# Kernel optimization log

Hardware: AMD Instinct MI355X
Metric: run time of the kernel (lower is better)

Reference implementation:

```python
import jax, jax.numpy as jnp
import numpy as np

TWO_PI = 2.0 * np.pi
B, S_IN, S_OUT, K, HID = 1024, 4096, 4096, 8, 512
EPS = 1e-6


def setup_inputs() -> dict:
    key = jax.random.key(0)
    k1, k2, k3, k4, k5, k6, k7, k8 = jax.random.split(key, 8)
    x_in = jax.random.uniform(k1, (B, S_OUT), dtype=jnp.float32) * TWO_PI
    x_passive = jax.random.normal(k2, (B, S_IN), dtype=jnp.float32)
    log_density = jax.random.normal(k3, (B, 1), dtype=jnp.float32)
    # MLP params (nn.Linear default-ish init scale)
    lim1 = 1.0 / np.sqrt(S_IN)
    lim2 = 1.0 / np.sqrt(HID)
    w1 = jax.random.uniform(k4, (S_IN, HID), jnp.float32, -lim1, lim1)
    b1 = jax.random.uniform(k5, (HID,), jnp.float32, -lim1, lim1)
    w2 = jax.random.uniform(k6, (HID, S_OUT * 3 * K), jnp.float32, -lim2, lim2)
    b2 = jax.random.uniform(k7, (S_OUT * 3 * K,), jnp.float32, -lim2, lim2)
    phase_shift = jax.random.uniform(k8, (1,), jnp.float32)
    return {"x_in": x_in, "x_passive": x_passive, "log_density": log_density,
            "w1": w1, "b1": b1, "w2": w2, "b2": b2, "phase_shift": phase_shift}


def reference(x_in, x_passive, log_density, w1, b1, w2, b2, phase_shift):
    # normalise network input with global mean / (unbiased) std, as torch does
    xn = (x_passive - x_passive.mean()) / x_passive.std(ddof=1)
    # dense network: Linear -> tanh -> Linear -> tanh (final_activation=activation)
    net = jnp.tanh(jnp.tanh(xn @ w1 + b1) @ w2 + b2)            # (B, S*3K)
    net = net.reshape(-1, S_OUT, 3 * K)
    h_raw, w_raw, d_raw = net[..., :K], net[..., K:2 * K], net[..., 2 * K:]
    h_norm = jax.nn.softmax(h_raw, axis=2) * TWO_PI              # (B,S,K)
    w_norm = jax.nn.softmax(w_raw, axis=2) * TWO_PI
    d_norm = jax.nn.softplus(d_raw)
    bshape = (h_norm.shape[0], S_OUT, 1)
    x_kp = jnp.concatenate([jnp.full(bshape, -EPS, h_norm.dtype),
                            jnp.cumsum(w_norm, axis=2)], axis=2)  # (B,S,K+1)
    phi_kp = jnp.concatenate([jnp.zeros(bshape, h_norm.dtype),
                              jnp.cumsum(h_norm, axis=2)], axis=2)
    x = x_in[..., None]                                          # (B,S,1)
    # searchsorted (left) per element: count of knots strictly less than x, minus 1
    k_ind = jnp.sum(x_kp < x, axis=2, keepdims=True) - 1         # (B,S,1) int
    k_ind = jnp.clip(k_ind, 0, K - 1)
    g = lambda a, i: jnp.take_along_axis(a, i, axis=2)
    w_k = g(w_norm, k_ind)
    h_k = g(h_norm, k_ind)
    s_k = h_k / w_k
    d_k = g(d_norm, k_ind)
    d_kp1 = g(d_norm, (k_ind + 1) % K)
    x_km1 = g(x_kp, k_ind)
    phi_km1 = g(phi_kp, k_ind)
    alpha = (x - x_km1) / w_k
    a1m = alpha * (1.0 - alpha)
    denom = s_k + (d_kp1 + d_k - 2.0 * s_k) * a1m
    phi_out = (phi_km1 + h_k * (s_k * alpha ** 2 + d_k * a1m) / denom)[..., 0]
    phi_out = (phi_out + phase_shift) % TWO_PI                   # (B,S)
    grad = s_k ** 2 * (d_kp1 * alpha ** 2 + 2.0 * s_k * a1m
                       + d_k * (1.0 - alpha) ** 2) / denom ** 2  # (B,S,1)
    log_density = log_density - jnp.log(grad).sum(axis=1)        # (B,1)
    return phi_out, log_density
```

## Files before the change

kernel.cpp:

```cpp
#include <hip/hip_runtime.h>
#include <cstdint>
#include <cstddef>


typedef unsigned short u16;
typedef __bf16 bf16x8 __attribute__((ext_vector_type(8)));
typedef float f32x4 __attribute__((ext_vector_type(4)));
typedef unsigned short u16x8 __attribute__((ext_vector_type(8)));
typedef unsigned short u16x4 __attribute__((ext_vector_type(4)));
typedef unsigned short u16x2 __attribute__((ext_vector_type(2)));

#define TWOPI_F 6.28318530717958647692f

static __device__ __forceinline__ u16 f32_to_bf16(float f){
  unsigned u = __builtin_bit_cast(unsigned, f);
  return (u16)((u + 0x7fffu + ((u >> 16) & 1u)) >> 16);
}
static __device__ __forceinline__ void async16(void* lds, const void* g){
  __builtin_amdgcn_global_load_lds((const __attribute__((address_space(1))) void*)g,
                                   (__attribute__((address_space(3))) void*)lds,
                                   16, 0, 0);
}
static __device__ __forceinline__ float fast_tanh(float x){
  x = fminf(fmaxf(x, -15.f), 15.f);
  float e = __expf(2.f * x);
  return (e - 1.f) / (e + 1.f);
}
static __device__ __forceinline__ float softplus_f(float x){
  return fmaxf(x, 0.f) + __logf(1.f + __expf(-fabsf(x)));
}

__global__ void k_stats(const float* __restrict__ xp, float* __restrict__ stats){
  __shared__ float ss[4], sq[4];
  const int tid = threadIdx.x;
  const long gt = (long)blockIdx.x * 256 + tid;
  const float4* x4 = (const float4*)xp;
  float s = 0.f, q = 0.f;
  #pragma unroll
  for (int p = 0; p < 4; ++p){
    float4 v = x4[gt + (long)p * 262144];
    s += v.x + v.y + v.z + v.w;
    q += v.x*v.x + v.y*v.y + v.z*v.z + v.w*v.w;
  }
  #pragma unroll
  for (int off = 32; off; off >>= 1){
    s += __shfl_down(s, off);
    q += __shfl_down(q, off);
  }
  if ((tid & 63) == 0){ ss[tid>>6] = s; sq[tid>>6] = q; }
  __syncthreads();
  if (tid == 0){
    atomicAdd(stats,     ss[0]+ss[1]+ss[2]+ss[3]);
    atomicAdd(stats + 1, sq[0]+sq[1]+sq[2]+sq[3]);
  }
}

__global__ void k_prep(const float* __restrict__ xp, const float* __restrict__ stats,
                       u16* __restrict__ xn){
  const long t = (long)blockIdx.x * 256 + threadIdx.x;
  const float sum = stats[0], sq = stats[1];
  const float N = 4194304.f;
  const float mean = sum / N;
  const float istd = rsqrtf((sq - sum*sum/N) / (N - 1.f));
  const float4* x4 = (const float4*)xp;
  const float4 a = x4[2*t], b = x4[2*t+1];
  u16x8 o;
  o[0]=f32_to_bf16((a.x-mean)*istd); o[1]=f32_to_bf16((a.y-mean)*istd);
  o[2]=f32_to_bf16((a.z-mean)*istd); o[3]=f32_to_bf16((a.w-mean)*istd);
  o[4]=f32_to_bf16((b.x-mean)*istd); o[5]=f32_to_bf16((b.y-mean)*istd);
  o[6]=f32_to_bf16((b.z-mean)*istd); o[7]=f32_to_bf16((b.w-mean)*istd);
  ((u16x8*)xn)[t] = o;
}

__global__ __launch_bounds__(256) void k_transpose_cvt(const float* __restrict__ in,
                                                       u16* __restrict__ out,
                                                       int Kd, int Nd){
  __shared__ __align__(16) u16 tT[128*256];
  const int tid = threadIdx.x;
  const long k0 = (long)blockIdx.x * 256, n0 = (long)blockIdx.y * 128;
  const int lam = tid & 31, g = tid >> 5;
  const int c = lam * 4;
  const int sig = (lam & 7) << 2;
  #pragma unroll
  for (int pass = 0; pass < 16; ++pass){
    const int P = pass*8 + g;
    const float4 f0 = *(const float4*)&in[(k0 + 2*P    )*Nd + n0 + c];
    const float4 f1 = *(const float4*)&in[(k0 + 2*P + 1)*Nd + n0 + c];
    const int pp = 2*(P ^ sig);
    *(u16x2*)&tT[(c    )*256 + pp] = u16x2{f32_to_bf16(f0.x), f32_to_bf16(f1.x)};
    *(u16x2*)&tT[(c + 1)*256 + pp] = u16x2{f32_to_bf16(f0.y), f32_to_bf16(f1.y)};
    *(u16x2*)&tT[(c + 2)*256 + pp] = u16x2{f32_to_bf16(f0.z), f32_to_bf16(f1.z)};
    *(u16x2*)&tT[(c + 3)*256 + pp] = u16x2{f32_to_bf16(f0.w), f32_to_bf16(f1.w)};
  }
  __syncthreads();
  const int w = tid >> 6, l = tid & 63;
  const int lh = l >> 5, lk = l & 31;
  #pragma unroll
  for (int it = 0; it < 16; ++it){
    const int n = (w << 5) + (it << 1) + lh;
    const int s2 = (n >> 2) & 7;
    const u16x8 v = *(const u16x8*)&tT[n*256 + 8*(lk ^ s2)];
    *(u16x8*)&out[(n0 + n)*Kd + k0 + 8*lk] = v;
  }
}

__global__ __launch_bounds__(256, 2) void k_gemm1(
    const u16* __restrict__ xn,
    const u16* __restrict__ w1t,
    float* __restrict__ pp)
{
  __shared__ __align__(16) u16 sA[64*32];
  __shared__ __align__(16) u16 sB[64*32];
  const int tid = threadIdx.x, lane = tid & 63, w = tid >> 6;
  const int n0 = blockIdx.x << 6, m0 = blockIdx.y << 6;
  const int ks = blockIdx.z;
  const int wm = w >> 1, wn = w & 1;
  const int rA = lane >> 2, cA = (lane & 3) << 3;
  const int fr = lane & 15, fq = lane >> 4;
  const f32x4 z4 = {0.f, 0.f, 0.f, 0.f};
  f32x4 acc[2][2];
  #pragma unroll
  for (int i=0;i<2;i++){ acc[i][0] = z4; acc[i][1] = z4; }

  for (int kt = 0; kt < 64; ++kt){
    const int kofs = (ks << 11) + (kt << 5) + cA;
    async16(sA + w*512, xn  + (long)(m0 + w*16 + rA)*4096 + kofs);
    async16(sB + w*512, w1t + (long)(n0 + w*16 + rA)*4096 + kofs);
    __syncthreads();
    bf16x8 af[2], bfv[2];
    #pragma unroll
    for (int i=0;i<2;i++) af[i]  = *(const bf16x8*)(sA + ((wm<<5) + i*16 + fr)*32 + (fq<<3));
    #pragma unroll
    for (int j=0;j<2;j++) bfv[j] = *(const bf16x8*)(sB + ((wn<<5) + j*16 + fr)*32 + (fq<<3));
    #pragma unroll
    for (int i=0;i<2;i++)
      #pragma unroll
      for (int j=0;j<2;j++)
        acc[i][j] = __builtin_amdgcn_mfma_f32_16x16x32_bf16(af[i], bfv[j], acc[i][j], 0, 0, 0);
    __syncthreads();
  }
  float* po = pp + ((size_t)ks << 19);
  #pragma unroll
  for (int i=0;i<2;i++)
    #pragma unroll
    for (int j=0;j<2;j++)
      #pragma unroll
      for (int r=0;r<4;r++){
        const int row = m0 + (wm<<5) + i*16 + (fq<<2) + r;
        const int col = n0 + (wn<<5) + j*16 + fr;
        po[row*512 + col] = acc[i][j][r];
      }
}

__global__ void k_gemm1b(const float* __restrict__ pp, const float* __restrict__ b1,
                         u16* __restrict__ hb){
  const int t = blockIdx.x * 256 + threadIdx.x;
  const float4 a = ((const float4*)pp)[t];
  const float4 b = ((const float4*)pp)[131072 + t];
  const float4 bb = ((const float4*)b1)[t & 127];
  u16x4 o;
  o[0] = f32_to_bf16(fast_tanh(a.x + b.x + bb.x));
  o[1] = f32_to_bf16(fast_tanh(a.y + b.y + bb.y));
  o[2] = f32_to_bf16(fast_tanh(a.z + b.z + bb.z));
  o[3] = f32_to_bf16(fast_tanh(a.w + b.w + bb.w));
  ((u16x4*)hb)[t] = o;
}

__global__ __launch_bounds__(256, 2) void k_gemm2(
    const u16* __restrict__ hmat,
    const u16* __restrict__ w2t,
    const float* __restrict__ b2,
    const float* __restrict__ x_in,
    const float* __restrict__ phase,
    float* __restrict__ phi_out,
    float* __restrict__ part)
{
  __shared__ __align__(16) char smem[25600];
  u16* sA = (u16*)smem;
  u16* sB = (u16*)(smem + 16384);
  float* sC = (float*)smem;

  const int tid  = threadIdx.x;
  const int lane = tid & 63;
  const int w    = tid >> 6;
  const int nt   = blockIdx.y;
  const int m0   = blockIdx.x << 8;
  const long n0  = (long)nt * 96;

  const int rA = lane >> 2, cA = (lane & 3) << 3;
  const int fr = lane & 15, fq = lane >> 4;

  const f32x4 z4 = {0.f, 0.f, 0.f, 0.f};
  f32x4 acc[4][6];
  #pragma unroll
  for (int i=0;i<4;i++)
    #pragma unroll
    for (int j=0;j<6;j++) acc[i][j] = z4;

  for (int kt = 0; kt < 16; ++kt){
    const int kofs = (kt << 5) + cA;
    #pragma unroll
    for (int cc = 0; cc < 4; ++cc){
      const int c = (w << 2) + cc;
      async16(sA + c*512, hmat + (long)(m0 + c*16 + rA)*512 + kofs);
    }
    #pragma unroll
    for (int cc = 0; cc < 2; ++cc){
      const int ch = (w << 1) + cc;
      int row = ch*16 + rA; if (row > 95) row = 95;
      async16(sB + ch*512, w2t + (n0 + row)*512 + kofs);
    }
    __syncthreads();
    bf16x8 af[4], bfv[6];
    #pragma unroll
    for (int i=0;i<4;i++)
      af[i] = *(const bf16x8*)(sA + ((w<<6) + i*16 + fr)*32 + (fq<<3));
    #pragma unroll
    for (int j=0;j<6;j++)
      bfv[j] = *(const bf16x8*)(sB + (j*16 + fr)*32 + (fq<<3));
    #pragma unroll
    for (int i=0;i<4;i++)
      #pragma unroll
      for (int j=0;j<6;j++)
        acc[i][j] = __builtin_amdgcn_mfma_f32_16x16x32_bf16(af[i], bfv[j], acc[i][j], 0, 0, 0);
    __syncthreads();
  }

  const float shift = phase[0];
  float b2c[6];
  #pragma unroll
  for (int j=0;j<6;j++) b2c[j] = b2[n0 + j*16 + fr];
  float* myC = sC + w*1600;

  #pragma unroll
  for (int q = 0; q < 4; ++q){
    __syncthreads();
    #pragma unroll
    for (int j=0;j<6;j++)
      #pragma unroll
      for (int r=0;r<4;r++)
        myC[((fq<<2)+r)*100 + j*16 + fr] = fast_tanh(acc[q][j][r] + b2c[j]);
    __syncthreads();

    const int row = fr;
    const int g   = fq;
    const float* tp = myC + row*100 + g*24;
    float t[24];
    #pragma unroll
    for (int jj=0;jj<24;jj++) t[jj] = tp[jj];

    const int bg = m0 + (w<<6) + (q<<4) + row;
    const int s  = (nt<<2) + g;
    const float x = x_in[(long)bg*4096 + s];

    float eh[8], ew[8];
    float sh = 0.f, sw = 0.f;
    #pragma unroll
    for (int i=0;i<8;i++){ eh[i] = __expf(t[i]);   sh += eh[i]; }
    #pragma unroll
    for (int i=0;i<8;i++){ ew[i] = __expf(t[8+i]); sw += ew[i]; }
    const float fh = TWOPI_F / sh, fw = TWOPI_F / sw;

    float cw = 0.f; int k = 0;
    #pragma unroll
    for (int i=0;i<8;i++){ cw += ew[i]*fw; k += (cw < x) ? 1 : 0; }
    if (k > 7) k = 7;

    float xkm1 = -1e-6f, ph = 0.f, wk = 0.f, hk = 0.f, dr0 = 0.f, dr1 = 0.f;
    float cw2 = 0.f, chs = 0.f;
    #pragma unroll
    for (int i=0;i<8;i++){
      const float wi = ew[i]*fw, hi = eh[i]*fh;
      if (i == k){
        wk = wi; hk = hi;
        xkm1 = (i == 0) ? -1e-6f : cw2;
        ph = chs;
        dr0 = t[16 + i];
        dr1 = t[16 + ((i+1)&7)];
      }
      cw2 += wi; chs += hi;
    }
    const float dk  = softplus_f(dr0);
    const float dk1 = softplus_f(dr1);
    const float sk  = hk / wk;
    const float alpha = (x - xkm1) / wk;
    const float a1m = alpha * (1.f - alpha);
    const float denom = sk + (dk1 + dk - 2.f*sk)*a1m;
    const float phiv = ph + hk*(sk*alpha*alpha + dk*a1m)/denom;
    float p = phiv + shift;
    if (p >= TWOPI_F) p -= TWOPI_F;
    if (p >= TWOPI_F) p -= TWOPI_F;
    phi_out[(long)bg*4096 + s] = p;

    const float om = 1.f - alpha;
    const float num = dk1*alpha*alpha + 2.f*sk*a1m + dk*om*om;
    float lg = __logf(sk*sk*num/(denom*denom));
    lg += __shfl_xor(lg, 16);
    lg += __shfl_xor(lg, 32);
    if (lane < 16) part[(long)bg*1024 + nt] = lg;
  }
}

__global__ void k_ldred(const float* __restrict__ part, const float* __restrict__ ldin,
                        float* __restrict__ ldout){
  __shared__ float ss[4];
  const int b = blockIdx.x, tid = threadIdx.x;
  const float4* p4 = (const float4*)(part + ((long)b << 10));
  const float4 v = p4[tid];
  float s = v.x + v.y + v.z + v.w;
  #pragma unroll
  for (int off = 32; off; off >>= 1) s += __shfl_down(s, off);
  if ((tid & 63) == 0) ss[tid >> 6] = s;
  __syncthreads();
  if (tid == 0) ldout[b] = ldin[b] - (ss[0]+ss[1]+ss[2]+ss[3]);
}

extern "C" void kernel_launch(void* const* d_in, const int* in_sizes, int n_in,
                              void* d_out, int out_size, void* d_ws, size_t ws_size,
                              hipStream_t stream){
  (void)in_sizes; (void)n_in; (void)out_size; (void)ws_size;
  const float* x_in  = (const float*)d_in[0];
  const float* x_pas = (const float*)d_in[1];
  const float* ldin  = (const float*)d_in[2];
  const float* w1    = (const float*)d_in[3];
  const float* b1    = (const float*)d_in[4];
  const float* w2    = (const float*)d_in[5];
  const float* b2    = (const float*)d_in[6];
  const float* phase = (const float*)d_in[7];
  float* out   = (float*)d_out;
  float* phi   = out;
  float* ldout = out + (size_t)1024*4096;

  char* ws = (char*)d_ws;
  float* stats = (float*)ws;
  u16* xn   = (u16*)(ws + 256);
  u16* w1t  = (u16*)(ws + 8388864);
  u16* hb   = (u16*)(ws + 12583168);
  u16* w2t  = (u16*)(ws + 13631744);
  float* part = (float*)(ws + 114295040);

  hipMemsetAsync(stats, 0, 8, stream);
  k_stats<<<1024, 256, 0, stream>>>(x_pas, stats);
  k_prep<<<2048, 256, 0, stream>>>(x_pas, stats, xn);
  k_transpose_cvt<<<dim3(16, 4),  256, 0, stream>>>(w1, w1t, 4096, 512);
  k_transpose_cvt<<<dim3(2, 768), 256, 0, stream>>>(w2, w2t, 512, 98304);
  k_gemm1<<<dim3(8, 16, 2), 256, 0, stream>>>(xn, w1t, part);
  k_gemm1b<<<512, 256, 0, stream>>>(part, b1, hb);
  k_gemm2<<<dim3(4, 1024), 256, 0, stream>>>(hb, w2t, b2, x_in, phase, phi, part);
  k_ldred<<<1024, 256, 0, stream>>>(part, ldin, ldout);
}
```

Baseline: 569.1 us.

## Loop over M tiles per block in gemm2 with wider K step and swizzled LDS

The second GEMM now launches one block per N tile and loops over the four 256-row M tiles inside the block, instead of launching a 4x1024 grid. The K step doubles to 64 with an XOR-swizzled LDS layout meant to avoid bank conflicts, and the row mapping is reshaped to 8-row chunks, which also removes the padded B-row clamp. The goals are fewer K-loop barriers, fewer blocks to schedule, and conflict-free LDS fragment reads. In exchange the kernel needs more LDS (44 KB), which may lower occupancy, and gets only 1024 blocks with a serial M loop, so it has less parallelism and may re-read the w2t tile once per M tile.

```diff
diff --git a/kernel.cpp b/kernel.cpp
--- a/kernel.cpp
+++ b/kernel.cpp
@@ -175,56 +175,21 @@
     float* __restrict__ phi_out,
     float* __restrict__ part)
 {
-  __shared__ __align__(16) char smem[25600];
+  __shared__ __align__(16) char smem[45056];
   u16* sA = (u16*)smem;
-  u16* sB = (u16*)(smem + 16384);
+  u16* sB = (u16*)(smem + 32768);
   float* sC = (float*)smem;
 
   const int tid  = threadIdx.x;
   const int lane = tid & 63;
   const int w    = tid >> 6;
-  const int nt   = blockIdx.y;
-  const int m0   = blockIdx.x << 8;
+  const int nt   = blockIdx.x;
   const long n0  = (long)nt * 96;
 
-  const int rA = lane >> 2, cA = (lane & 3) << 3;
   const int fr = lane & 15, fq = lane >> 4;
-
-  const f32x4 z4 = {0.f, 0.f, 0.f, 0.f};
-  f32x4 acc[4][6];
-  #pragma unroll
-  for (int i=0;i<4;i++)
-    #pragma unroll
-    for (int j=0;j<6;j++) acc[i][j] = z4;
-
-  for (int kt = 0; kt < 16; ++kt){
-    const int kofs = (kt << 5) + cA;
-    #pragma unroll
-    for (int cc = 0; cc < 4; ++cc){
-      const int c = (w << 2) + cc;
-      async16(sA + c*512, hmat + (long)(m0 + c*16 + rA)*512 + kofs);
-    }
-    #pragma unroll
-    for (int cc = 0; cc < 2; ++cc){
-      const int ch = (w << 1) + cc;
-      int row = ch*16 + rA; if (row > 95) row = 95;
-      async16(sB + ch*512, w2t + (n0 + row)*512 + kofs);
-    }
-    __syncthreads();
-    bf16x8 af[4], bfv[6];
-    #pragma unroll
-    for (int i=0;i<4;i++)
-      af[i] = *(const bf16x8*)(sA + ((w<<6) + i*16 + fr)*32 + (fq<<3));
-    #pragma unroll
-    for (int j=0;j<6;j++)
-      bfv[j] = *(const bf16x8*)(sB + (j*16 + fr)*32 + (fq<<3));
-    #pragma unroll
-    for (int i=0;i<4;i++)
-      #pragma unroll
-      for (int j=0;j<6;j++)
-        acc[i][j] = __builtin_amdgcn_mfma_f32_16x16x32_bf16(af[i], bfv[j], acc[i][j], 0, 0, 0);
-    __syncthreads();
-  }
+  const int lr = lane >> 3;
+  const int gch = ((lane & 7) ^ (lr & 7)) << 3;
+  const int swz = fr & 7;
 
   const float shift = phase[0];
   float b2c[6];
@@ -232,72 +197,115 @@
   for (int j=0;j<6;j++) b2c[j] = b2[n0 + j*16 + fr];
   float* myC = sC + w*1600;
 
-  #pragma unroll
-  for (int q = 0; q < 4; ++q){
-    __syncthreads();
-    #pragma unroll
-    for (int j=0;j<6;j++)
-      #pragma unroll
-      for (int r=0;r<4;r++)
-        myC[((fq<<2)+r)*100 + j*16 + fr] = fast_tanh(acc[q][j][r] + b2c[j]);
-    __syncthreads();
-
-    const int row = fr;
-    const int g   = fq;
-    const float* tp = myC + row*100 + g*24;
-    float t[24];
-    #pragma unroll
-    for (int jj=0;jj<24;jj++) t[jj] = tp[jj];
-
-    const int bg = m0 + (w<<6) + (q<<4) + row;
-    const int s  = (nt<<2) + g;
-    const float x = x_in[(long)bg*4096 + s];
-
-    float eh[8], ew[8];
-    float sh = 0.f, sw = 0.f;
-    #pragma unroll
-    for (int i=0;i<8;i++){ eh[i] = __expf(t[i]);   sh += eh[i]; }
-    #pragma unroll
-    for (int i=0;i<8;i++){ ew[i] = __expf(t[8+i]); sw += ew[i]; }
-    const float fh = TWOPI_F / sh, fw = TWOPI_F / sw;
-
-    float cw = 0.f; int k = 0;
-    #pragma unroll
-    for (int i=0;i<8;i++){ cw += ew[i]*fw; k += (cw < x) ? 1 : 0; }
-    if (k > 7) k = 7;
-
-    float xkm1 = -1e-6f, ph = 0.f, wk = 0.f, hk = 0.f, dr0 = 0.f, dr1 = 0.f;
-    float cw2 = 0.f, chs = 0.f;
-    #pragma unroll
-    for (int i=0;i<8;i++){
-      const float wi = ew[i]*fw, hi = eh[i]*fh;
-      if (i == k){
-        wk = wi; hk = hi;
-        xkm1 = (i == 0) ? -1e-6f : cw2;
-        ph = chs;
-        dr0 = t[16 + i];
-        dr1 = t[16 + ((i+1)&7)];
-      }
-      cw2 += wi; chs += hi;
+  const f32x4 z4 = {0.f, 0.f, 0.f, 0.f};
+
+  for (int mt = 0; mt < 4; ++mt){
+    const int m0 = mt << 8;
+    f32x4 acc[4][6];
+    #pragma unroll
+    for (int i=0;i<4;i++)
+      #pragma unroll
+      for (int j=0;j<6;j++) acc[i][j] = z4;
+
+    for (int kt = 0; kt < 8; ++kt){
+      const int kofs = (kt << 6) + gch;
+      #pragma unroll
+      for (int i = 0; i < 8; ++i){
+        const int a = (w << 3) + i;
+        async16(sA + a*512, hmat + (long)(m0 + a*8 + lr)*512 + kofs);
+      }
+      #pragma unroll
+      for (int i = 0; i < 3; ++i){
+        const int b = w*3 + i;
+        async16(sB + b*512, w2t + (n0 + b*8 + lr)*512 + kofs);
+      }
+      __syncthreads();
+      #pragma unroll
+      for (int h = 0; h < 2; ++h){
+        const int ch = (((h<<2) + fq) ^ swz) << 3;
+        bf16x8 af[4], bfv[6];
+        #pragma unroll
+        for (int i=0;i<4;i++)
+          af[i] = *(const bf16x8*)(sA + ((w<<6) + i*16 + fr)*64 + ch);
+        #pragma unroll
+        for (int j=0;j<6;j++)
+          bfv[j] = *(const bf16x8*)(sB + (j*16 + fr)*64 + ch);
+        #pragma unroll
+        for (int i=0;i<4;i++)
+          #pragma unroll
+          for (int j=0;j<6;j++)
+            acc[i][j] = __builtin_amdgcn_mfma_f32_16x16x32_bf16(af[i], bfv[j], acc[i][j], 0, 0, 0);
+      }
+      __syncthreads();
     }
-    const float dk  = softplus_f(dr0);
-    const float dk1 = softplus_f(dr1);
-    const float sk  = hk / wk;
-    const float alpha = (x - xkm1) / wk;
-    const float a1m = alpha * (1.f - alpha);
-    const float denom = sk + (dk1 + dk - 2.f*sk)*a1m;
-    const float phiv = ph + hk*(sk*alpha*alpha + dk*a1m)/denom;
-    float p = phiv + shift;
-    if (p >= TWOPI_F) p -= TWOPI_F;
-    if (p >= TWOPI_F) p -= TWOPI_F;
-    phi_out[(long)bg*4096 + s] = p;
-
-    const float om = 1.f - alpha;
-    const float num = dk1*alpha*alpha + 2.f*sk*a1m + dk*om*om;
-    float lg = __logf(sk*sk*num/(denom*denom));
-    lg += __shfl_xor(lg, 16);
-    lg += __shfl_xor(lg, 32);
-    if (lane < 16) part[(long)bg*1024 + nt] = lg;
+
+    #pragma unroll
+    for (int q = 0; q < 4; ++q){
+      #pragma unroll
+      for (int j=0;j<6;j++)
+        #pragma unroll
+        for (int r=0;r<4;r++)
+          myC[((fq<<2)+r)*100 + j*16 + fr] = fast_tanh(acc[q][j][r] + b2c[j]);
+      __syncthreads();
+
+      const int row = fr;
+      const int g   = fq & 3;
+      const float* tp = myC + row*100 + g*24;
+      float t[24];
+      #pragma unroll
+      for (int jj=0;jj<24;jj++) t[jj] = tp[jj];
+
+      const int bg = m0 + (w<<6) + (q<<4) + row;
+      const int s  = (nt<<2) + g;
+      const float x = x_in[(long)bg*4096 + s];
+
+      float eh[8], ew[8];
+      float sh = 0.f, sw = 0.f;
+      #pragma unroll
+      for (int i=0;i<8;i++){ eh[i] = __expf(t[i]);   sh += eh[i]; }
+      #pragma unroll
+      for (int i=0;i<8;i++){ ew[i] = __expf(t[8+i]); sw += ew[i]; }
+      const float fh = TWOPI_F / sh, fw = TWOPI_F / sw;
+
+      float cw = 0.f; int k = 0;
+      #pragma unroll
+      for (int i=0;i<8;i++){ cw += ew[i]*fw; k += (cw < x) ? 1 : 0; }
+      if (k > 7) k = 7;
+
+      float xkm1 = -1e-6f, ph = 0.f, wk = 0.f, hk = 0.f, dr0 = 0.f, dr1 = 0.f;
+      float cw2 = 0.f, chs = 0.f;
+      #pragma unroll
+      for (int i=0;i<8;i++){
+        const float wi = ew[i]*fw, hi = eh[i]*fh;
+        if (i == k){
+          wk = wi; hk = hi;
+          xkm1 = (i == 0) ? -1e-6f : cw2;
+          ph = chs;
+          dr0 = t[16 + i];
+          dr1 = t[16 + ((i+1)&7)];
+        }
+        cw2 += wi; chs += hi;
+      }
+      const float dk  = softplus_f(dr0);
+      const float dk1 = softplus_f(dr1);
+      const float sk  = hk / wk;
+      const float alpha = (x - xkm1) / wk;
+      const float a1m = alpha * (1.f - alpha);
+      const float denom = sk + (dk1 + dk - 2.f*sk)*a1m;
+      const float phiv = ph + hk*(sk*alpha*alpha + dk*a1m)/denom;
+      float p = phiv + shift;
+      if (p >= TWOPI_F) p -= TWOPI_F;
+      if (p >= TWOPI_F) p -= TWOPI_F;
+      phi_out[(long)bg*4096 + s] = p;
+
+      const float om = 1.f - alpha;
+      const float num = dk1*alpha*alpha + 2.f*sk*a1m + dk*om*om;
+      float lg = __logf(sk*sk*num/(denom*denom));
+      lg += __shfl_xor(lg, 16);
+      lg += __shfl_xor(lg, 32);
+      if (lane < 16) part[(long)bg*1024 + nt] = lg;
+      __syncthreads();
+    }
   }
 }
 
@@ -346,6 +354,6 @@
   k_transpose_cvt<<<dim3(2, 768), 256, 0, stream>>>(w2, w2t, 512, 98304);
   k_gemm1<<<dim3(8, 16, 2), 256, 0, stream>>>(xn, w1t, part);
   k_gemm1b<<<512, 256, 0, stream>>>(part, b1, hb);
-  k_gemm2<<<dim3(4, 1024), 256, 0, stream>>>(hb, w2t, b2, x_in, phase, phi, part);
+  k_gemm2<<<1024, 256, 0, stream>>>(hb, w2t, b2, x_in, phase, phi, part);
   k_ldred<<<1024, 256, 0, stream>>>(part, ldin, ldout);
 }
```

Result: slower. 583.3 us (+2.5%).
